# Kernel optimization log

Hardware: AMD Instinct MI355X
Metric: run time of the kernel (lower is better)

The kernel has to match this reference:

```python
import jax, jax.numpy as jnp
import numpy as np

H = 2048
NH = 16
DH = H // NH
EPS = 1e-05


def setup_inputs() -> dict:
    key = jax.random.key(0)
    ks = jax.random.split(key, 12)
    B, S, A = 4, 2048, 512
    s = 1.0 / np.sqrt(H)
    inp = {
        "hidden_states": jax.random.normal(ks[0], (B, S, H), jnp.float32),
        "audio_tokens": jax.random.normal(ks[1], (B, A, H), jnp.float32),
        "attention_mask": jax.random.randint(ks[2], (B, A), 0, 2).astype(jnp.float32),
        "Wq": jax.random.normal(ks[3], (H, H), jnp.float32) * s,
        "bq": jnp.zeros((H,), jnp.float32),
        "Wk": jax.random.normal(ks[4], (H, H), jnp.float32) * s,
        "bk": jnp.zeros((H,), jnp.float32),
        "Wv": jax.random.normal(ks[5], (H, H), jnp.float32) * s,
        "bv": jnp.zeros((H,), jnp.float32),
        "Wo": jax.random.normal(ks[6], (H, H), jnp.float32) * s,
        "bo": jnp.zeros((H,), jnp.float32),
        "gamma": jnp.ones((H,), jnp.float32),
        "beta": jnp.zeros((H,), jnp.float32),
    }
    return inp


def reference(hidden_states, audio_tokens, attention_mask,
              Wq, bq, Wk, bk, Wv, bv, Wo, bo, gamma, beta):
    B, S, _ = hidden_states.shape
    A = audio_tokens.shape[1]
    # projections (weights stored [in, out])
    q = (hidden_states @ Wq + bq).reshape(B, S, NH, DH)
    k = (audio_tokens @ Wk + bk).reshape(B, A, NH, DH)
    v = (audio_tokens @ Wv + bv).reshape(B, A, NH, DH)
    # scores: [B, NH, S, A]
    scores = jnp.einsum('bqhd,bkhd->bhqk', q, k) / np.sqrt(DH)
    scores = scores + attention_mask[:, None, None, :] * -10000.0
    probs = jax.nn.softmax(scores, axis=-1)
    # context: [B, S, NH, DH] -> [B, S, H]
    ctx = jnp.einsum('bhqk,bkhd->bqhd', probs, v).reshape(B, S, H)
    out = ctx @ Wo + bo
    # residual + LayerNorm
    x = out + hidden_states
    mu = jnp.mean(x, axis=-1, keepdims=True)
    var = jnp.mean(jnp.square(x - mu), axis=-1, keepdims=True)
    return (x - mu) * jax.lax.rsqrt(var + EPS) * gamma + beta
```

## Files before the change

### kernel.cpp

```cpp
#include <hip/hip_runtime.h>

#define HDIM 2048
#define NHEAD 16
#define DHEAD 128
#define BATCH 4
#define SEQ 2048
#define AUD 512

typedef unsigned short u16;
typedef unsigned int u32;
typedef __bf16 bf16_t;
typedef bf16_t bf16x8 __attribute__((ext_vector_type(8)));
typedef short short8 __attribute__((ext_vector_type(8)));
typedef float f32x4 __attribute__((ext_vector_type(4)));

typedef const __attribute__((address_space(1))) u32 gas_u32;
typedef __attribute__((address_space(3))) u32 las_u32;

__device__ __forceinline__ float b2f(u16 h) {
  union { u32 u; float f; } v; v.u = ((u32)h) << 16; return v.f;
}
__device__ __forceinline__ u16 f2b(float f) {
  union { float f; u32 u; } v; v.f = f;
  u32 r = (v.u + 0x7FFFu + ((v.u >> 16) & 1u)) >> 16;
  return (u16)r;
}

__global__ __launch_bounds__(256) void cvt2_k(const float* __restrict__ s0,
                                              u16* __restrict__ d0, int n0,
                                              const float* __restrict__ s1,
                                              u16* __restrict__ d1, int n1) {
  int i = blockIdx.x * 256 + threadIdx.x;
  const float* src; u16* dst; int j;
  if (i < n0) { src = s0; dst = d0; j = i; }
  else { j = i - n0; if (j >= n1) return; src = s1; dst = d1; }
  const float4* s4 = (const float4*)src;
  float4 a = s4[2 * j], b = s4[2 * j + 1];
  short8 o;
  o[0] = (short)f2b(a.x); o[1] = (short)f2b(a.y);
  o[2] = (short)f2b(a.z); o[3] = (short)f2b(a.w);
  o[4] = (short)f2b(b.x); o[5] = (short)f2b(b.y);
  o[6] = (short)f2b(b.z); o[7] = (short)f2b(b.w);
  *(short8*)(dst + (size_t)j * 8) = o;
}

__global__ __launch_bounds__(256) void transpose4_k(
    const float* __restrict__ Wq, const float* __restrict__ Wk,
    const float* __restrict__ Wv, const float* __restrict__ Wo,
    u16* __restrict__ dst4) {
  const float* src = (blockIdx.z == 0) ? Wq
                   : (blockIdx.z == 1) ? Wk
                   : (blockIdx.z == 2) ? Wv : Wo;
  u16* dst = dst4 + (size_t)blockIdx.z * HDIM * HDIM;
  __shared__ float tile[32][33];
  int tx = threadIdx.x, ty = threadIdx.y;
  int x = blockIdx.x * 32 + tx;
  int y0 = blockIdx.y * 32;
#pragma unroll
  for (int j = 0; j < 32; j += 8)
    tile[ty + j][tx] = src[(size_t)(y0 + ty + j) * HDIM + x];
  __syncthreads();
  int x2 = y0 + tx;
  int y2 = blockIdx.x * 32;
#pragma unroll
  for (int j = 0; j < 32; j += 8)
    dst[(size_t)(y2 + ty + j) * HDIM + x2] = f2b(tile[tx][ty + j]);
}

__global__ __launch_bounds__(256) void gemm_bt(
    const u16* __restrict__ A, int lda,
    const u16* __restrict__ Bt, int ldb,
    void* __restrict__ Cv, int ldc,
    const float* __restrict__ bias, float alpha, int M, int N, int K, int cmode) {
  __shared__ u16 As[128 * 32];
  __shared__ u16 Bs[128 * 32];

  int lane = threadIdx.x & 63;
  int wave = threadIdx.x >> 6;
  int gdx = gridDim.x;
  int id = blockIdx.y * gdx + blockIdx.x;
  int cpx = (gdx * gridDim.y) >> 3;
  int sid = (id & 7) * cpx + (id >> 3);
  int m0 = (sid / gdx) * 128;
  int n0 = (sid % gdx) * 128;
  int wm = (wave & 1) * 64;
  int wn = (wave >> 1) * 64;
  int row16 = lane & 15;
  int quad = lane >> 4;

  int sr = (lane >> 2);
  int sc = (lane & 3) * 8;

  f32x4 acc[4][4];
#pragma unroll
  for (int i = 0; i < 4; i++)
#pragma unroll
    for (int j = 0; j < 4; j++) acc[i][j] = (f32x4){0.f, 0.f, 0.f, 0.f};

  for (int k0 = 0; k0 < K; k0 += 32) {
#pragma unroll
    for (int t = 0; t < 2; t++) {
      int chunk = wave * 2 + t;
      int r = chunk * 16 + sr;
      const u16* ga = A + (size_t)(m0 + r) * lda + k0 + sc;
      const u16* gb = Bt + (size_t)(n0 + r) * ldb + k0 + sc;
      __builtin_amdgcn_global_load_lds((gas_u32*)ga, (las_u32*)(As + chunk * 512), 16, 0, 0);
      __builtin_amdgcn_global_load_lds((gas_u32*)gb, (las_u32*)(Bs + chunk * 512), 16, 0, 0);
    }
    __syncthreads();

    short8 af[4], bf[4];
#pragma unroll
    for (int mt = 0; mt < 4; mt++)
      af[mt] = *(const short8*)(As + (wm + mt * 16 + row16) * 32 + quad * 8);
#pragma unroll
    for (int nt = 0; nt < 4; nt++)
      bf[nt] = *(const short8*)(Bs + (wn + nt * 16 + row16) * 32 + quad * 8);
#pragma unroll
    for (int mt = 0; mt < 4; mt++)
#pragma unroll
      for (int nt = 0; nt < 4; nt++)
        acc[mt][nt] = __builtin_amdgcn_mfma_f32_16x16x32_bf16(
            __builtin_bit_cast(bf16x8, af[mt]), __builtin_bit_cast(bf16x8, bf[nt]),
            acc[mt][nt], 0, 0, 0);
    __syncthreads();
  }

#pragma unroll
  for (int nt = 0; nt < 4; nt++) {
    int nn = n0 + wn + nt * 16 + row16;
    float bv = bias ? bias[nn] : 0.f;
#pragma unroll
    for (int mt = 0; mt < 4; mt++) {
#pragma unroll
      for (int r = 0; r < 4; r++) {
        int mm = m0 + wm + mt * 16 + quad * 4 + r;
        float val = (acc[mt][nt][r] + bv) * alpha;
        if (cmode == 2) {
          ((float*)Cv)[(size_t)mm * ldc + nn] = val;
        } else if (cmode == 1) {
          int bb = mm >> 9, aa = mm & 511;
          int hh = nn >> 7, dd = nn & 127;
          ((u16*)Cv)[((size_t)((bb * 16 + hh) * 128 + dd)) * 512 + aa] = f2b(val);
        } else {
          ((u16*)Cv)[(size_t)mm * ldc + nn] = f2b(val);
        }
      }
    }
  }
}

__global__ __launch_bounds__(512, 2) void gemm_ring(
    const u16* __restrict__ A, int lda,
    const u16* __restrict__ Bt, int ldb,
    void* __restrict__ Cv, int ldc,
    const float* __restrict__ bias, float alpha, int K, int cmode) {
  __shared__ u16 As[3][256 * 64];
  __shared__ u16 Bs[3][128 * 64];

  int tid = threadIdx.x;
  int lane = tid & 63, wave = tid >> 6;
  int wr = wave >> 1, wc = wave & 1;
  int row16 = lane & 15, quad = lane >> 4;
  int swr = (row16 & 7) << 3;

  int gdx = gridDim.x;
  int id = blockIdx.y * gdx + blockIdx.x;
  int cpx = (gdx * gridDim.y) >> 3;
  int sid = (id & 7) * cpx + (id >> 3);
  int n0 = (sid % gdx) * 128;
  int m0 = (sid / gdx) * 256;

  f32x4 acc[4][4];
#pragma unroll
  for (int i = 0; i < 4; i++)
#pragma unroll
    for (int j = 0; j < 4; j++) acc[i][j] = (f32x4){0.f, 0.f, 0.f, 0.f};

  auto stage = [&](int slot, int k0) {
#pragma unroll
    for (int l = 0; l < 4; l++) {
      int d = l * 512 + tid;
      int row = d >> 3;
      int csw = ((d & 7) ^ (row & 7)) << 3;
      __builtin_amdgcn_global_load_lds(
          (gas_u32*)(A + (size_t)(m0 + row) * lda + k0 + csw),
          (las_u32*)(&As[slot][d * 8]), 16, 0, 0);
    }
#pragma unroll
    for (int l = 0; l < 2; l++) {
      int d = l * 512 + tid;
      int row = d >> 3;
      int csw = ((d & 7) ^ (row & 7)) << 3;
      __builtin_amdgcn_global_load_lds(
          (gas_u32*)(Bt + (size_t)(n0 + row) * ldb + k0 + csw),
          (las_u32*)(&Bs[slot][d * 8]), 16, 0, 0);
    }
  };

  auto compute = [&](int slot) {
#pragma unroll
    for (int kk = 0; kk < 2; kk++) {
      int cof = (kk * 32 + quad * 8) ^ swr;
      short8 af[4], bfr[4];
#pragma unroll
      for (int mi = 0; mi < 4; mi++)
        af[mi] = *(const short8*)(&As[slot][(wr * 64 + mi * 16 + row16) * 64 + cof]);
#pragma unroll
      for (int ni = 0; ni < 4; ni++)
        bfr[ni] = *(const short8*)(&Bs[slot][(wc * 64 + ni * 16 + row16) * 64 + cof]);
#pragma unroll
      for (int mi = 0; mi < 4; mi++)
#pragma unroll
        for (int ni = 0; ni < 4; ni++)
          acc[mi][ni] = __builtin_amdgcn_mfma_f32_16x16x32_bf16(
              __builtin_bit_cast(bf16x8, af[mi]), __builtin_bit_cast(bf16x8, bfr[ni]),
              acc[mi][ni], 0, 0, 0);
    }
  };

  int NT = K >> 6;
  stage(0, 0);
  stage(1, 64);
  asm volatile("s_waitcnt vmcnt(6)" ::: "memory");
  __builtin_amdgcn_s_barrier();

  int slot = 0;
  for (int kt = 0; kt < NT; ++kt) {
    int s2 = slot + 2; if (s2 >= 3) s2 -= 3;
    if (kt + 2 < NT) stage(s2, (kt + 2) << 6);
    compute(slot);
    if (kt + 2 < NT) {
      asm volatile("s_waitcnt vmcnt(6) lgkmcnt(0)" ::: "memory");
    } else {
      asm volatile("s_waitcnt vmcnt(0) lgkmcnt(0)" ::: "memory");
    }
    __builtin_amdgcn_s_barrier();
    slot++; if (slot >= 3) slot -= 3;
  }

#pragma unroll
  for (int ni = 0; ni < 4; ni++) {
    int nn = n0 + wc * 64 + ni * 16 + row16;
    float bv = bias ? bias[nn] : 0.f;
#pragma unroll
    for (int mi = 0; mi < 4; mi++) {
#pragma unroll
      for (int r = 0; r < 4; r++) {
        int mm = m0 + wr * 64 + mi * 16 + quad * 4 + r;
        float val = (acc[mi][ni][r] + bv) * alpha;
        if (cmode == 2) ((float*)Cv)[(size_t)mm * ldc + nn] = val;
        else            ((u16*)Cv)[(size_t)mm * ldc + nn] = f2b(val);
      }
    }
  }
}

__global__ __launch_bounds__(256) void flash_k(
    const u16* __restrict__ Q, const u16* __restrict__ K,
    const u16* __restrict__ Vt, const float* __restrict__ mask,
    u16* __restrict__ Ctx) {
  __shared__ u16 KP[128 * 128];
  __shared__ u16 Vs[128 * 128];

  int bh = blockIdx.y, b = bh >> 4, h = bh & 15;
  int q0 = blockIdx.x * 128;
  int lane = threadIdx.x & 63, wave = threadIdx.x >> 6;
  int row16 = lane & 15, quad = lane >> 4;
  int wq = wave * 32;
  int swr = (row16 & 7) << 3;

  const u16* qbase = Q + ((size_t)(b * SEQ + q0)) * HDIM + h * DHEAD;
  const u16* kbase = K + ((size_t)b * AUD) * HDIM + h * DHEAD;
  const u16* vbase = Vt + ((size_t)(b * NHEAD + h)) * DHEAD * AUD;
  const float* mp = mask + b * AUD;

  short8 qf[2][4];
#pragma unroll
  for (int mt = 0; mt < 2; mt++)
#pragma unroll
    for (int ks = 0; ks < 4; ks++)
      qf[mt][ks] = *(const short8*)(qbase + (size_t)(wq + mt * 16 + row16) * HDIM +
                                    ks * 32 + quad * 8);

  f32x4 oacc[2][8];
  float lacc[2][4];
#pragma unroll
  for (int mt = 0; mt < 2; mt++) {
#pragma unroll
    for (int nt = 0; nt < 8; nt++) oacc[mt][nt] = (f32x4){0.f, 0.f, 0.f, 0.f};
#pragma unroll
    for (int r = 0; r < 4; r++) lacc[mt][r] = 0.f;
  }

  int sl = (lane >> 4);
  int scol = (lane & 15) * 8;

  for (int kt = 0; kt < 4; kt++) {
#pragma unroll
    for (int t = 0; t < 8; t++) {
      int c = wave * 8 + t;
      int r = c * 4 + sl;
      int csw = scol ^ ((r & 7) << 3);
      __builtin_amdgcn_global_load_lds(
          (gas_u32*)(kbase + (size_t)(kt * 128 + r) * HDIM + csw),
          (las_u32*)(KP + c * 512), 16, 0, 0);
      __builtin_amdgcn_global_load_lds(
          (gas_u32*)(vbase + (size_t)r * AUD + kt * 128 + csw),
          (las_u32*)(Vs + c * 512), 16, 0, 0);
    }
    __syncthreads();

    f32x4 sacc[2][8];
#pragma unroll
    for (int mt = 0; mt < 2; mt++)
#pragma unroll
      for (int nt = 0; nt < 8; nt++) sacc[mt][nt] = (f32x4){0.f, 0.f, 0.f, 0.f};
#pragma unroll
    for (int ks = 0; ks < 4; ks++) {
      short8 bf[8];
      int cofs = (ks * 32 + quad * 8) ^ swr;
#pragma unroll
      for (int nt = 0; nt < 8; nt++)
        bf[nt] = *(const short8*)(KP + (nt * 16 + row16) * 128 + cofs);
#pragma unroll
      for (int mt = 0; mt < 2; mt++)
#pragma unroll
        for (int nt = 0; nt < 8; nt++)
          sacc[mt][nt] = __builtin_amdgcn_mfma_f32_16x16x32_bf16(
              __builtin_bit_cast(bf16x8, qf[mt][ks]), __builtin_bit_cast(bf16x8, bf[nt]),
              sacc[mt][nt], 0, 0, 0);
    }

#pragma unroll
    for (int nt = 0; nt < 8; nt++) {
      float mval = mp[kt * 128 + nt * 16 + row16] * (-10000.0f);
#pragma unroll
      for (int mt = 0; mt < 2; mt++)
#pragma unroll
        for (int r = 0; r < 4; r++) {
          float e = __expf(sacc[mt][nt][r] + mval);
          sacc[mt][nt][r] = e;
          lacc[mt][r] += e;
        }
    }
    __syncthreads();

#pragma unroll
    for (int mt = 0; mt < 2; mt++)
#pragma unroll
      for (int nt = 0; nt < 8; nt++)
#pragma unroll
        for (int r = 0; r < 4; r++) {
          int prow = wq + mt * 16 + quad * 4 + r;
          KP[prow * 128 + ((nt * 16 + row16) ^ ((prow & 7) << 3))] =
              f2b(sacc[mt][nt][r]);
        }
    __syncthreads();

#pragma unroll
    for (int ks = 0; ks < 4; ks++) {
      short8 af[2], bf[8];
      int cofs = (ks * 32 + quad * 8) ^ swr;
#pragma unroll
      for (int mt = 0; mt < 2; mt++)
        af[mt] = *(const short8*)(KP + (wq + mt * 16 + row16) * 128 + cofs);
#pragma unroll
      for (int nt = 0; nt < 8; nt++)
        bf[nt] = *(const short8*)(Vs + (nt * 16 + row16) * 128 + cofs);
#pragma unroll
      for (int mt = 0; mt < 2; mt++)
#pragma unroll
        for (int nt = 0; nt < 8; nt++)
          oacc[mt][nt] = __builtin_amdgcn_mfma_f32_16x16x32_bf16(
              __builtin_bit_cast(bf16x8, af[mt]), __builtin_bit_cast(bf16x8, bf[nt]),
              oacc[mt][nt], 0, 0, 0);
    }
    __syncthreads();
  }

#pragma unroll
  for (int mt = 0; mt < 2; mt++)
#pragma unroll
    for (int r = 0; r < 4; r++) {
      float s = lacc[mt][r];
      for (int off = 1; off < 16; off <<= 1) s += __shfl_xor(s, off, 64);
      lacc[mt][r] = 1.0f / s;
    }

  u16* cb = Ctx + ((size_t)(b * SEQ + q0 + wq)) * HDIM + h * DHEAD;
#pragma unroll
  for (int mt = 0; mt < 2; mt++)
#pragma unroll
    for (int nt = 0; nt < 8; nt++)
#pragma unroll
      for (int r = 0; r < 4; r++)
        cb[(size_t)(mt * 16 + quad * 4 + r) * HDIM + nt * 16 + row16] =
            f2b(oacc[mt][nt][r] * lacc[mt][r]);
}

__global__ __launch_bounds__(256) void ln_k(const float* O,
                                            const float* __restrict__ hs,
                                            const float* __restrict__ gamma,
                                            const float* __restrict__ beta,
                                            float* out) {
  size_t rowoff = (size_t)blockIdx.x * HDIM;
  float x[8], sum = 0.f, sq = 0.f;
#pragma unroll
  for (int i = 0; i < 8; i++) {
    int idx = threadIdx.x + 256 * i;
    float v = O[rowoff + idx] + hs[rowoff + idx];
    x[i] = v;
    sum += v;
    sq += v * v;
  }
  for (int off = 32; off; off >>= 1) {
    sum += __shfl_xor(sum, off, 64);
    sq += __shfl_xor(sq, off, 64);
  }
  __shared__ float red[8];
  int wave = threadIdx.x >> 6, lane = threadIdx.x & 63;
  if (lane == 0) { red[wave] = sum; red[4 + wave] = sq; }
  __syncthreads();
  sum = red[0] + red[1] + red[2] + red[3];
  sq = red[4] + red[5] + red[6] + red[7];
  float mu = sum * (1.0f / HDIM);
  float var = sq * (1.0f / HDIM) - mu * mu;
  float inv = rsqrtf(var + 1e-5f);
#pragma unroll
  for (int i = 0; i < 8; i++) {
    int idx = threadIdx.x + 256 * i;
    out[rowoff + idx] = (x[i] - mu) * inv * gamma[idx] + beta[idx];
  }
}

extern "C" void kernel_launch(void* const* d_in, const int* in_sizes, int n_in,
                              void* d_out, int out_size, void* d_ws, size_t ws_size,
                              hipStream_t stream) {
  (void)in_sizes; (void)n_in; (void)out_size; (void)ws_size;
  const float* hs   = (const float*)d_in[0];
  const float* at   = (const float*)d_in[1];
  const float* mask = (const float*)d_in[2];
  const float* Wq = (const float*)d_in[3];  const float* bq = (const float*)d_in[4];
  const float* Wk = (const float*)d_in[5];  const float* bk = (const float*)d_in[6];
  const float* Wv = (const float*)d_in[7];  const float* bv = (const float*)d_in[8];
  const float* Wo = (const float*)d_in[9];  const float* bo = (const float*)d_in[10];
  const float* gamma = (const float*)d_in[11];
  const float* beta  = (const float*)d_in[12];
  float* out = (float*)d_out;
  u16* ws = (u16*)d_ws;

  u16* hsb = ws;
  u16* atb = ws + 16777216;
  u16* wT4 = ws + 20971520;
  u16* Q   = ws + 37748736;
  u16* Kb  = ws + 54525952;
  u16* Vt  = ws + 58720256;
  u16* Ctx = ws + 62914560;
  u16* wTq = wT4;
  u16* wTk = wT4 + 4194304;
  u16* wTv = wT4 + 8388608;
  u16* wTo = wT4 + 12582912;

  cvt2_k<<<10240, 256, 0, stream>>>(hs, hsb, 2097152, at, atb, 524288);
  transpose4_k<<<dim3(64, 64, 4), dim3(32, 8), 0, stream>>>(Wq, Wk, Wv, Wo, wT4);

  const float qscale = 0.08838834764831845f;

  gemm_ring<<<dim3(16, 32), 512, 0, stream>>>(hsb, HDIM, wTq, HDIM, Q, HDIM,
                                              bq, qscale, 2048, 0);
  gemm_bt<<<dim3(16, 16), 256, 0, stream>>>(atb, HDIM, wTk, HDIM, Kb, HDIM,
                                            bk, 1.0f, 2048, 2048, 2048, 0);
  gemm_bt<<<dim3(16, 16), 256, 0, stream>>>(atb, HDIM, wTv, HDIM, Vt, HDIM,
                                            bv, 1.0f, 2048, 2048, 2048, 1);

  flash_k<<<dim3(SEQ / 128, BATCH * NHEAD), 256, 0, stream>>>(Q, Kb, Vt, mask, Ctx);

  gemm_ring<<<dim3(16, 32), 512, 0, stream>>>(Ctx, HDIM, wTo, HDIM, out, HDIM,
                                              bo, 1.0f, 2048, 2);
  ln_k<<<8192, 256, 0, stream>>>(out, hs, gamma, beta, out);
}
```

Baseline: 611.0 us.

## Use 256x256 GEMM tiles with 4-stage K=32 pipeline and MFMA priority

Replaces the 256x128 triple-buffered GEMM with a 256x256 tile kernel that uses K-steps of 32 and a 4-slot LDS ring. Each K-step is split into two half-compute phases, with the A and B prefetches interleaved between them under explicit waitcnt and barrier control. s_setprio is raised around MFMA bursts here and in the flash attention kernel. The aim is more data reuse per block and better overlap of loads with compute. The cost is more accumulator registers, half as many blocks (256) on the device, and more barriers per step.

After: 594.4 us. -2.7%, faster.

```diff
diff --git a/kernel.cpp b/kernel.cpp
--- a/kernel.cpp
+++ b/kernel.cpp
@@ -150,93 +150,113 @@
   }
 }
 
-__global__ __launch_bounds__(512, 2) void gemm_ring(
+__global__ __launch_bounds__(512, 2) void gemm_ring8(
     const u16* __restrict__ A, int lda,
     const u16* __restrict__ Bt, int ldb,
     void* __restrict__ Cv, int ldc,
     const float* __restrict__ bias, float alpha, int K, int cmode) {
-  __shared__ u16 As[3][256 * 64];
-  __shared__ u16 Bs[3][128 * 64];
+  __shared__ u16 As[4][256 * 32];
+  __shared__ u16 Bs[4][256 * 32];
 
   int tid = threadIdx.x;
   int lane = tid & 63, wave = tid >> 6;
-  int wr = wave >> 1, wc = wave & 1;
+  int wr = wave >> 2, wc = wave & 3;
   int row16 = lane & 15, quad = lane >> 4;
-  int swr = (row16 & 7) << 3;
+  int cofs = (quad * 8) ^ (((row16 >> 1) & 3) << 3);
 
   int gdx = gridDim.x;
   int id = blockIdx.y * gdx + blockIdx.x;
   int cpx = (gdx * gridDim.y) >> 3;
   int sid = (id & 7) * cpx + (id >> 3);
-  int n0 = (sid % gdx) * 128;
+  int n0 = (sid % gdx) * 256;
   int m0 = (sid / gdx) * 256;
 
-  f32x4 acc[4][4];
-#pragma unroll
-  for (int i = 0; i < 4; i++)
+  int r0 = tid >> 2;
+  int c0 = ((tid & 3) ^ ((r0 >> 1) & 3)) * 8;
+
+  f32x4 acc[8][4];
+#pragma unroll
+  for (int i = 0; i < 8; i++)
 #pragma unroll
     for (int j = 0; j < 4; j++) acc[i][j] = (f32x4){0.f, 0.f, 0.f, 0.f};
 
-  auto stage = [&](int slot, int k0) {
-#pragma unroll
-    for (int l = 0; l < 4; l++) {
-      int d = l * 512 + tid;
-      int row = d >> 3;
-      int csw = ((d & 7) ^ (row & 7)) << 3;
+  auto stageA = [&](int slot, int k0) {
+#pragma unroll
+    for (int l = 0; l < 2; l++) {
+      int row = l * 128 + r0;
       __builtin_amdgcn_global_load_lds(
-          (gas_u32*)(A + (size_t)(m0 + row) * lda + k0 + csw),
-          (las_u32*)(&As[slot][d * 8]), 16, 0, 0);
-    }
+          (gas_u32*)(A + (size_t)(m0 + row) * lda + k0 + c0),
+          (las_u32*)(&As[slot][(l * 512 + tid) * 8]), 16, 0, 0);
+    }
+  };
+  auto stageB = [&](int slot, int k0) {
 #pragma unroll
     for (int l = 0; l < 2; l++) {
-      int d = l * 512 + tid;
-      int row = d >> 3;
-      int csw = ((d & 7) ^ (row & 7)) << 3;
+      int row = l * 128 + r0;
       __builtin_amdgcn_global_load_lds(
-          (gas_u32*)(Bt + (size_t)(n0 + row) * ldb + k0 + csw),
-          (las_u32*)(&Bs[slot][d * 8]), 16, 0, 0);
+          (gas_u32*)(Bt + (size_t)(n0 + row) * ldb + k0 + c0),
+          (las_u32*)(&Bs[slot][(l * 512 + tid) * 8]), 16, 0, 0);
     }
   };
 
-  auto compute = [&](int slot) {
-#pragma unroll
-    for (int kk = 0; kk < 2; kk++) {
-      int cof = (kk * 32 + quad * 8) ^ swr;
-      short8 af[4], bfr[4];
-#pragma unroll
-      for (int mi = 0; mi < 4; mi++)
-        af[mi] = *(const short8*)(&As[slot][(wr * 64 + mi * 16 + row16) * 64 + cof]);
+  int NT = K >> 5;
+  stageA(0, 0);  stageB(0, 0);
+  stageA(1, 32); stageB(1, 32);
+  stageA(2, 64); stageB(2, 64);
+  asm volatile("s_waitcnt vmcnt(8)" ::: "memory");
+  __builtin_amdgcn_s_barrier();
+
+  for (int kt = 0; kt < NT; ++kt) {
+    int slot = kt & 3;
+    int sp = (kt + 3) & 3;
+    bool pf = (kt + 3) < NT;
+    const u16* as = &As[slot][0];
+    const u16* bs = &Bs[slot][0];
+
+    short8 bfr[4], af[4];
+#pragma unroll
+    for (int ni = 0; ni < 4; ni++)
+      bfr[ni] = *(const short8*)(bs + (wc * 64 + ni * 16 + row16) * 32 + cofs);
+#pragma unroll
+    for (int mi = 0; mi < 4; mi++)
+      af[mi] = *(const short8*)(as + (wr * 128 + mi * 16 + row16) * 32 + cofs);
+    if (pf) stageA(sp, (kt + 3) << 5);
+    __builtin_amdgcn_s_barrier();
+    asm volatile("s_waitcnt lgkmcnt(0)" ::: "memory");
+    __builtin_amdgcn_s_setprio(1);
+#pragma unroll
+    for (int mi = 0; mi < 4; mi++)
 #pragma unroll
       for (int ni = 0; ni < 4; ni++)
-        bfr[ni] = *(const short8*)(&Bs[slot][(wc * 64 + ni * 16 + row16) * 64 + cof]);
-#pragma unroll
-      for (int mi = 0; mi < 4; mi++)
-#pragma unroll
-        for (int ni = 0; ni < 4; ni++)
-          acc[mi][ni] = __builtin_amdgcn_mfma_f32_16x16x32_bf16(
-              __builtin_bit_cast(bf16x8, af[mi]), __builtin_bit_cast(bf16x8, bfr[ni]),
-              acc[mi][ni], 0, 0, 0);
-    }
-  };
-
-  int NT = K >> 6;
-  stage(0, 0);
-  stage(1, 64);
-  asm volatile("s_waitcnt vmcnt(6)" ::: "memory");
-  __builtin_amdgcn_s_barrier();
-
-  int slot = 0;
-  for (int kt = 0; kt < NT; ++kt) {
-    int s2 = slot + 2; if (s2 >= 3) s2 -= 3;
-    if (kt + 2 < NT) stage(s2, (kt + 2) << 6);
-    compute(slot);
-    if (kt + 2 < NT) {
-      asm volatile("s_waitcnt vmcnt(6) lgkmcnt(0)" ::: "memory");
-    } else {
-      asm volatile("s_waitcnt vmcnt(0) lgkmcnt(0)" ::: "memory");
-    }
+        acc[mi][ni] = __builtin_amdgcn_mfma_f32_16x16x32_bf16(
+            __builtin_bit_cast(bf16x8, af[mi]), __builtin_bit_cast(bf16x8, bfr[ni]),
+            acc[mi][ni], 0, 0, 0);
+    __builtin_amdgcn_s_setprio(0);
     __builtin_amdgcn_s_barrier();
-    slot++; if (slot >= 3) slot -= 3;
+
+    short8 ag[4];
+#pragma unroll
+    for (int mi = 0; mi < 4; mi++)
+      ag[mi] = *(const short8*)(as + (wr * 128 + (mi + 4) * 16 + row16) * 32 + cofs);
+    if (pf) stageB(sp, (kt + 3) << 5);
+    {
+      int nf = NT - 2 - kt;
+      if (nf >= 2)      asm volatile("s_waitcnt vmcnt(8)" ::: "memory");
+      else if (nf == 1) asm volatile("s_waitcnt vmcnt(4)" ::: "memory");
+      else              asm volatile("s_waitcnt vmcnt(0)" ::: "memory");
+    }
+    __builtin_amdgcn_s_barrier();
+    asm volatile("s_waitcnt lgkmcnt(0)" ::: "memory");
+    __builtin_amdgcn_s_setprio(1);
+#pragma unroll
+    for (int mi = 0; mi < 4; mi++)
+#pragma unroll
+      for (int ni = 0; ni < 4; ni++)
+        acc[mi + 4][ni] = __builtin_amdgcn_mfma_f32_16x16x32_bf16(
+            __builtin_bit_cast(bf16x8, ag[mi]), __builtin_bit_cast(bf16x8, bfr[ni]),
+            acc[mi + 4][ni], 0, 0, 0);
+    __builtin_amdgcn_s_setprio(0);
+    __builtin_amdgcn_s_barrier();
   }
 
 #pragma unroll
@@ -244,10 +264,10 @@
     int nn = n0 + wc * 64 + ni * 16 + row16;
     float bv = bias ? bias[nn] : 0.f;
 #pragma unroll
-    for (int mi = 0; mi < 4; mi++) {
+    for (int mi = 0; mi < 8; mi++) {
 #pragma unroll
       for (int r = 0; r < 4; r++) {
-        int mm = m0 + wr * 64 + mi * 16 + quad * 4 + r;
+        int mm = m0 + wr * 128 + mi * 16 + quad * 4 + r;
         float val = (acc[mi][ni][r] + bv) * alpha;
         if (cmode == 2) ((float*)Cv)[(size_t)mm * ldc + nn] = val;
         else            ((u16*)Cv)[(size_t)mm * ldc + nn] = f2b(val);
@@ -323,6 +343,7 @@
 #pragma unroll
       for (int nt = 0; nt < 8; nt++)
         bf[nt] = *(const short8*)(KP + (nt * 16 + row16) * 128 + cofs);
+      __builtin_amdgcn_s_setprio(1);
 #pragma unroll
       for (int mt = 0; mt < 2; mt++)
 #pragma unroll
@@ -330,6 +351,7 @@
           sacc[mt][nt] = __builtin_amdgcn_mfma_f32_16x16x32_bf16(
               __builtin_bit_cast(bf16x8, qf[mt][ks]), __builtin_bit_cast(bf16x8, bf[nt]),
               sacc[mt][nt], 0, 0, 0);
+      __builtin_amdgcn_s_setprio(0);
     }
 
 #pragma unroll
@@ -368,6 +390,7 @@
 #pragma unroll
       for (int nt = 0; nt < 8; nt++)
         bf[nt] = *(const short8*)(Vs + (nt * 16 + row16) * 128 + cofs);
+      __builtin_amdgcn_s_setprio(1);
 #pragma unroll
       for (int mt = 0; mt < 2; mt++)
 #pragma unroll
@@ -375,6 +398,7 @@
           oacc[mt][nt] = __builtin_amdgcn_mfma_f32_16x16x32_bf16(
               __builtin_bit_cast(bf16x8, af[mt]), __builtin_bit_cast(bf16x8, bf[nt]),
               oacc[mt][nt], 0, 0, 0);
+      __builtin_amdgcn_s_setprio(0);
     }
     __syncthreads();
   }
@@ -467,7 +491,7 @@
 
   const float qscale = 0.08838834764831845f;
 
-  gemm_ring<<<dim3(16, 32), 512, 0, stream>>>(hsb, HDIM, wTq, HDIM, Q, HDIM,
+  gemm_ring8<<<dim3(8, 32), 512, 0, stream>>>(hsb, HDIM, wTq, HDIM, Q, HDIM,
                                               bq, qscale, 2048, 0);
   gemm_bt<<<dim3(16, 16), 256, 0, stream>>>(atb, HDIM, wTk, HDIM, Kb, HDIM,
                                             bk, 1.0f, 2048, 2048, 2048, 0);
@@ -476,7 +500,7 @@
 
   flash_k<<<dim3(SEQ / 128, BATCH * NHEAD), 256, 0, stream>>>(Q, Kb, Vt, mask, Ctx);
 
-  gemm_ring<<<dim3(16, 32), 512, 0, stream>>>(Ctx, HDIM, wTo, HDIM, out, HDIM,
+  gemm_ring8<<<dim3(8, 32), 512, 0, stream>>>(Ctx, HDIM, wTo, HDIM, out, HDIM,
                                               bo, 1.0f, 2048, 2);
   ln_k<<<8192, 256, 0, stream>>>(out, hs, gamma, beta, out);
 }
```
